# Kernel tuning notes

Hardware: AMD Instinct MI355X
Metric: run time of the kernel (lower is better)

Reference implementation:

```python
import jax, jax.numpy as jnp
import numpy as np

BATCH, N_SITES, BOND, PHYS = 4096, 1024, 32, 2
NOISE = 0.001  # keep trace of long product positive so log() is finite in fp32


def setup_inputs() -> dict:
    key = jax.random.key(0)
    k1, k2 = jax.random.split(key)
    s = jax.random.normal(k1, (BATCH, N_SITES), dtype=jnp.float32)
    # MPS tensor A[p] = I + small noise (same shapes/math as the module's param;
    # identity offset keeps the 1024-matrix product numerically benign)
    A = jnp.eye(BOND, dtype=jnp.float32)[None, :, :] + NOISE * jax.random.normal(
        k2, (PHYS, BOND, BOND), dtype=jnp.float32)
    return {"s": s, "A": A}


def reference(s, A):
    # s: [B, N] float; A: [phys, D, D]
    s_idx = (s > 0).astype(jnp.int32)               # phys_dim == 2 path: [B, N]
    B = s.shape[0]
    D = A.shape[-1]
    init = jnp.broadcast_to(jnp.eye(D, dtype=A.dtype), (B, D, D))

    def contract_site(carry, idx):
        # gather per-sample site matrix [B, D, D], batched matmul
        return jnp.matmul(carry, A[idx]), None

    final_prod, _ = jax.lax.scan(contract_site, init, s_idx.T)  # scan over N sites
    val = jnp.trace(final_prod, axis1=1, axis2=2)               # [B]
    return jnp.log(val)
```

## Files before the change

kernel.cpp:

```cpp
#include <hip/hip_runtime.h>
#include <hip/hip_bf16.h>


#define BATCH   4096
#define N_SITES 1024
#define NKEYS   256
#define NSTEP_H 64

typedef __attribute__((ext_vector_type(8)))  short    short8;
typedef __attribute__((ext_vector_type(16))) float    f32x16;
typedef __attribute__((ext_vector_type(4)))  unsigned uint4v;

static __device__ __forceinline__ unsigned short f32_to_bf16(float f) {
  unsigned u = __builtin_bit_cast(unsigned, f);
  const unsigned rounding = 0x7FFFu + ((u >> 16) & 1u);
  return (unsigned short)((u + rounding) >> 16);
}

static __device__ __forceinline__ unsigned cvt_pk_bf16(float lo, float hi) {
  unsigned r;
  asm("v_cvt_pk_bf16_f32 %0, %1, %2" : "=v"(r) : "v"(lo), "v"(hi));
  return r;
}

__global__ __launch_bounds__(256) void build_table_k(const float* __restrict__ A,
                                                     unsigned short* __restrict__ table) {
  __shared__ float As[2][32][32];
  __shared__ float M[2][32][32];
  const int key = blockIdx.x;
  const int t   = threadIdx.x;

  for (int i = t; i < 2 * 32 * 32; i += 256) ((float*)As)[i] = A[i];

  const int row = t >> 3;
  const int col = (t & 7) << 2;
  __syncthreads();

  {
    const int b0 = key & 1;
    const float4 v = *reinterpret_cast<const float4*>(&As[b0][row][col]);
    *reinterpret_cast<float4*>(&M[0][row][col]) = v;
  }
  __syncthreads();

  int cur = 0;
  for (int i = 1; i < 8; ++i) {
    const int bi = (key >> i) & 1;
    float a0 = 0.f, a1 = 0.f, a2 = 0.f, a3 = 0.f;
    for (int k = 0; k < 32; ++k) {
      const float m  = M[cur][row][k];
      const float4 v = *reinterpret_cast<const float4*>(&As[bi][k][col]);
      a0 += m * v.x; a1 += m * v.y; a2 += m * v.z; a3 += m * v.w;
    }
    M[cur ^ 1][row][col + 0] = a0;
    M[cur ^ 1][row][col + 1] = a1;
    M[cur ^ 1][row][col + 2] = a2;
    M[cur ^ 1][row][col + 3] = a3;
    __syncthreads();
    cur ^= 1;
  }

  const int c    = t >> 7;
  const int l    = (t >> 1) & 63;
  const int e4   = (t & 1) << 2;
  const int rowm = l & 31;
  const int hi   = l >> 5;

  unsigned long long packed = 0;
  for (int e = 0; e < 4; ++e) {
    const int ee = e4 + e;
    const int sg = (ee & 3) + ((ee >> 2) << 3) + (hi << 2) + (c << 4);
    const unsigned short us = f32_to_bf16(M[cur][sg][rowm]);
    packed |= (unsigned long long)us << (16 * e);
  }
  *reinterpret_cast<unsigned long long*>(table + (size_t)key * 1024 + c * 512 + l * 8 + e4) = packed;
}

__global__ __launch_bounds__(256) void mps_chain_k(const float* __restrict__ s,
                                                   const unsigned short* __restrict__ table,
                                                   float* __restrict__ out) {
  const int t    = threadIdx.x;
  const int pair = t >> 7;
  const int wv   = (t >> 6) & 1;
  const int lane = t & 63;
  const int b    = blockIdx.x * 2 + pair;

  __shared__ unsigned char keys[2][128 + 8];
  __shared__ float Ht[2][1024];

  const int kidx = wv * 64 + lane;
  const float4* s4 = reinterpret_cast<const float4*>(s) + (size_t)b * 256 + kidx * 2;
  const float4 va = s4[0];
  const float4 vb = s4[1];
  const unsigned key =
      (va.x > 0.f ? 1u : 0u)  | (va.y > 0.f ? 2u : 0u)  |
      (va.z > 0.f ? 4u : 0u)  | (va.w > 0.f ? 8u : 0u)  |
      (vb.x > 0.f ? 16u : 0u) | (vb.y > 0.f ? 32u : 0u) |
      (vb.z > 0.f ? 64u : 0u) | (vb.w > 0.f ? 128u : 0u);
  keys[pair][kidx] = (unsigned char)key;
  if (t < 16) keys[t >> 3][128 + (t & 7)] = 0;
  __syncthreads();

  const int col = lane & 31;
  const int hi  = lane >> 5;

  f32x16 acc;
#pragma unroll
  for (int r = 0; r < 16; ++r) {
    const int rr = (r & 3) + 8 * (r >> 2) + 4 * hi;
    acc[r] = (rr == col) ? 1.f : 0.f;
  }

  const unsigned char* kw = keys[pair] + wv * NSTEP_H;
  const unsigned long long laneoff = (unsigned long long)lane * 8;

  unsigned kA = kw[0], kB = kw[1];
  unsigned kC = kw[2];
  const unsigned short* e0 = table + (size_t)kA * 1024;
  const unsigned short* e1 = table + (size_t)kB * 1024;
  uint4v c0 = *reinterpret_cast<const uint4v*>(e0 + laneoff);
  uint4v c1 = *reinterpret_cast<const uint4v*>(e0 + 512 + laneoff);
  uint4v n0 = *reinterpret_cast<const uint4v*>(e1 + laneoff);
  uint4v n1 = *reinterpret_cast<const uint4v*>(e1 + 512 + laneoff);

#pragma unroll 4
  for (int j = 0; j < NSTEP_H; ++j) {
    const unsigned short* ef = table + ((size_t)kC << 10);
    const uint4v f0 = *reinterpret_cast<const uint4v*>(ef + laneoff);
    const uint4v f1 = *reinterpret_cast<const uint4v*>(ef + 512 + laneoff);
    kC = kw[j + 3];

    union { unsigned u[4]; short8 v; } B1, B2;
#pragma unroll
    for (int i = 0; i < 4; ++i) {
      B1.u[i] = cvt_pk_bf16(acc[2 * i],     acc[2 * i + 1]);
      B2.u[i] = cvt_pk_bf16(acc[8 + 2 * i], acc[9 + 2 * i]);
    }

    union { uint4v q; short8 v; } ua0, ua1;
    ua0.q = c0; ua1.q = c1;

    f32x16 z;
#pragma unroll
    for (int r = 0; r < 16; ++r) z[r] = 0.f;

    f32x16 t1 = __builtin_amdgcn_mfma_f32_32x32x16_bf16(ua0.v, B1.v, z, 0, 0, 0);
    acc = __builtin_amdgcn_mfma_f32_32x32x16_bf16(ua1.v, B2.v, t1, 0, 0, 0);
    asm("" : "+v"(acc));

    c0 = n0; c1 = n1; n0 = f0; n1 = f1;
  }

  if (wv == 1) {
#pragma unroll
    for (int r = 0; r < 16; ++r) {
      const int a = (r & 3) + 8 * (r >> 2) + 4 * hi;
      Ht[pair][col * 32 + ((a + col) & 31)] = acc[r];
    }
  }
  __syncthreads();
  if (wv == 0) {
    float dot = 0.f;
#pragma unroll
    for (int r = 0; r < 16; ++r) {
      const int k = (r & 3) + 8 * (r >> 2) + 4 * hi;
      dot += acc[r] * Ht[pair][k * 32 + ((col + k) & 31)];
    }
#pragma unroll
    for (int off = 32; off > 0; off >>= 1) dot += __shfl_down(dot, off, 64);
    if (lane == 0) out[b] = logf(dot);
  }
}

extern "C" void kernel_launch(void* const* d_in, const int* in_sizes, int n_in,
                              void* d_out, int out_size, void* d_ws, size_t ws_size,
                              hipStream_t stream) {
  const float* s = (const float*)d_in[0];
  const float* A = (const float*)d_in[1];
  float* out = (float*)d_out;
  unsigned short* table = (unsigned short*)d_ws;

  build_table_k<<<NKEYS, 256, 0, stream>>>(A, table);
  mps_chain_k<<<BATCH / 2, 256, 0, stream>>>(s, table, out);
}
```

Baseline: 118.7 us.

## Interleave two independent sample chains per wave to hide MFMA latency

Each wave now advances two samples' matrix chains at once, interleaving their MFMA and bf16 conversion steps so the two dependency chains overlap. Each block handles four samples instead of two, and the grid is halved. The aim is to hide the serial MFMA-to-convert latency of a single chain. In exchange each wave holds more registers and there are fewer blocks, which may lower occupancy.

```diff
diff --git a/kernel.cpp b/kernel.cpp
--- a/kernel.cpp
+++ b/kernel.cpp
@@ -80,95 +80,126 @@
                                                    const unsigned short* __restrict__ table,
                                                    float* __restrict__ out) {
   const int t    = threadIdx.x;
-  const int pair = t >> 7;
-  const int wv   = (t >> 6) & 1;
+  const int wave = t >> 6;
   const int lane = t & 63;
-  const int b    = blockIdx.x * 2 + pair;
-
-  __shared__ unsigned char keys[2][128 + 8];
-  __shared__ float Ht[2][1024];
-
-  const int kidx = wv * 64 + lane;
-  const float4* s4 = reinterpret_cast<const float4*>(s) + (size_t)b * 256 + kidx * 2;
-  const float4 va = s4[0];
-  const float4 vb = s4[1];
-  const unsigned key =
-      (va.x > 0.f ? 1u : 0u)  | (va.y > 0.f ? 2u : 0u)  |
-      (va.z > 0.f ? 4u : 0u)  | (va.w > 0.f ? 8u : 0u)  |
-      (vb.x > 0.f ? 16u : 0u) | (vb.y > 0.f ? 32u : 0u) |
-      (vb.z > 0.f ? 64u : 0u) | (vb.w > 0.f ? 128u : 0u);
-  keys[pair][kidx] = (unsigned char)key;
-  if (t < 16) keys[t >> 3][128 + (t & 7)] = 0;
+  const int half = wave & 1;
+  const int bA   = (wave >> 1) * 2;
+  const int bB   = bA + 1;
+
+  __shared__ unsigned char keys[4][136];
+  __shared__ float Ht[4][1024];
+
+#pragma unroll
+  for (int g = t; g < 512; g += 256) {
+    const int kb   = g >> 7;
+    const int kidx = g & 127;
+    const int bg   = blockIdx.x * 4 + kb;
+    const float4* s4 = reinterpret_cast<const float4*>(s) + (size_t)bg * 256 + kidx * 2;
+    const float4 va = s4[0];
+    const float4 vb = s4[1];
+    const unsigned key =
+        (va.x > 0.f ? 1u : 0u)  | (va.y > 0.f ? 2u : 0u)  |
+        (va.z > 0.f ? 4u : 0u)  | (va.w > 0.f ? 8u : 0u)  |
+        (vb.x > 0.f ? 16u : 0u) | (vb.y > 0.f ? 32u : 0u) |
+        (vb.z > 0.f ? 64u : 0u) | (vb.w > 0.f ? 128u : 0u);
+    keys[kb][kidx] = (unsigned char)key;
+  }
+  if (t < 32) keys[t >> 3][128 + (t & 7)] = 0;
   __syncthreads();
 
   const int col = lane & 31;
   const int hi  = lane >> 5;
 
-  f32x16 acc;
+  f32x16 accA, accB;
 #pragma unroll
   for (int r = 0; r < 16; ++r) {
     const int rr = (r & 3) + 8 * (r >> 2) + 4 * hi;
-    acc[r] = (rr == col) ? 1.f : 0.f;
-  }
-
-  const unsigned char* kw = keys[pair] + wv * NSTEP_H;
+    const float v = (rr == col) ? 1.f : 0.f;
+    accA[r] = v; accB[r] = v;
+  }
+
+  const unsigned char* kwA = &keys[bA][half * NSTEP_H];
+  const unsigned char* kwB = &keys[bB][half * NSTEP_H];
   const unsigned long long laneoff = (unsigned long long)lane * 8;
 
-  unsigned kA = kw[0], kB = kw[1];
-  unsigned kC = kw[2];
-  const unsigned short* e0 = table + (size_t)kA * 1024;
-  const unsigned short* e1 = table + (size_t)kB * 1024;
-  uint4v c0 = *reinterpret_cast<const uint4v*>(e0 + laneoff);
-  uint4v c1 = *reinterpret_cast<const uint4v*>(e0 + 512 + laneoff);
-  uint4v n0 = *reinterpret_cast<const uint4v*>(e1 + laneoff);
-  uint4v n1 = *reinterpret_cast<const uint4v*>(e1 + 512 + laneoff);
-
-#pragma unroll 4
+  const unsigned short* eA0 = table + ((size_t)kwA[0] << 10);
+  const unsigned short* eA1 = table + ((size_t)kwA[1] << 10);
+  const unsigned short* eB0 = table + ((size_t)kwB[0] << 10);
+  const unsigned short* eB1 = table + ((size_t)kwB[1] << 10);
+  unsigned kCA = kwA[2], kCB = kwB[2];
+  uint4v cA0 = *reinterpret_cast<const uint4v*>(eA0 + laneoff);
+  uint4v cA1 = *reinterpret_cast<const uint4v*>(eA0 + 512 + laneoff);
+  uint4v nA0 = *reinterpret_cast<const uint4v*>(eA1 + laneoff);
+  uint4v nA1 = *reinterpret_cast<const uint4v*>(eA1 + 512 + laneoff);
+  uint4v cB0 = *reinterpret_cast<const uint4v*>(eB0 + laneoff);
+  uint4v cB1 = *reinterpret_cast<const uint4v*>(eB0 + 512 + laneoff);
+  uint4v nB0 = *reinterpret_cast<const uint4v*>(eB1 + laneoff);
+  uint4v nB1 = *reinterpret_cast<const uint4v*>(eB1 + 512 + laneoff);
+
+#pragma unroll 2
   for (int j = 0; j < NSTEP_H; ++j) {
-    const unsigned short* ef = table + ((size_t)kC << 10);
-    const uint4v f0 = *reinterpret_cast<const uint4v*>(ef + laneoff);
-    const uint4v f1 = *reinterpret_cast<const uint4v*>(ef + 512 + laneoff);
-    kC = kw[j + 3];
-
-    union { unsigned u[4]; short8 v; } B1, B2;
+    const unsigned short* efA = table + ((size_t)kCA << 10);
+    const uint4v fA0 = *reinterpret_cast<const uint4v*>(efA + laneoff);
+    const uint4v fA1 = *reinterpret_cast<const uint4v*>(efA + 512 + laneoff);
+    kCA = kwA[j + 3];
+    const unsigned short* efB = table + ((size_t)kCB << 10);
+    const uint4v fB0 = *reinterpret_cast<const uint4v*>(efB + laneoff);
+    const uint4v fB1 = *reinterpret_cast<const uint4v*>(efB + 512 + laneoff);
+    kCB = kwB[j + 3];
+
+    f32x16 z;
+#pragma unroll
+    for (int r = 0; r < 16; ++r) z[r] = 0.f;
+
+    union { unsigned u[4]; short8 v; } BA1, BA2, BB1, BB2;
 #pragma unroll
     for (int i = 0; i < 4; ++i) {
-      B1.u[i] = cvt_pk_bf16(acc[2 * i],     acc[2 * i + 1]);
-      B2.u[i] = cvt_pk_bf16(acc[8 + 2 * i], acc[9 + 2 * i]);
-    }
-
-    union { uint4v q; short8 v; } ua0, ua1;
-    ua0.q = c0; ua1.q = c1;
-
-    f32x16 z;
-#pragma unroll
-    for (int r = 0; r < 16; ++r) z[r] = 0.f;
-
-    f32x16 t1 = __builtin_amdgcn_mfma_f32_32x32x16_bf16(ua0.v, B1.v, z, 0, 0, 0);
-    acc = __builtin_amdgcn_mfma_f32_32x32x16_bf16(ua1.v, B2.v, t1, 0, 0, 0);
-    asm("" : "+v"(acc));
-
-    c0 = n0; c1 = n1; n0 = f0; n1 = f1;
-  }
-
-  if (wv == 1) {
+      BA1.u[i] = cvt_pk_bf16(accA[2 * i],     accA[2 * i + 1]);
+      BA2.u[i] = cvt_pk_bf16(accA[8 + 2 * i], accA[9 + 2 * i]);
+      BB1.u[i] = cvt_pk_bf16(accB[2 * i],     accB[2 * i + 1]);
+      BB2.u[i] = cvt_pk_bf16(accB[8 + 2 * i], accB[9 + 2 * i]);
+    }
+
+    union { uint4v q; short8 v; } uA0, uA1, uB0, uB1;
+    uA0.q = cA0; uA1.q = cA1; uB0.q = cB0; uB1.q = cB1;
+
+    f32x16 tA = __builtin_amdgcn_mfma_f32_32x32x16_bf16(uA0.v, BA1.v, z, 0, 0, 0);
+    f32x16 tB = __builtin_amdgcn_mfma_f32_32x32x16_bf16(uB0.v, BB1.v, z, 0, 0, 0);
+    accA = __builtin_amdgcn_mfma_f32_32x32x16_bf16(uA1.v, BA2.v, tA, 0, 0, 0);
+    accB = __builtin_amdgcn_mfma_f32_32x32x16_bf16(uB1.v, BB2.v, tB, 0, 0, 0);
+
+    cA0 = nA0; cA1 = nA1; nA0 = fA0; nA1 = fA1;
+    cB0 = nB0; cB1 = nB1; nB0 = fB0; nB1 = fB1;
+  }
+
+  if (half == 1) {
 #pragma unroll
     for (int r = 0; r < 16; ++r) {
       const int a = (r & 3) + 8 * (r >> 2) + 4 * hi;
-      Ht[pair][col * 32 + ((a + col) & 31)] = acc[r];
-    }
-  }
-  __syncthreads();
-  if (wv == 0) {
-    float dot = 0.f;
+      const int slot = col * 32 + ((a + col) & 31);
+      Ht[bA][slot] = accA[r];
+      Ht[bB][slot] = accB[r];
+    }
+  }
+  __syncthreads();
+  if (half == 0) {
+    float d0 = 0.f, d1 = 0.f;
 #pragma unroll
     for (int r = 0; r < 16; ++r) {
       const int k = (r & 3) + 8 * (r >> 2) + 4 * hi;
-      dot += acc[r] * Ht[pair][k * 32 + ((col + k) & 31)];
-    }
-#pragma unroll
-    for (int off = 32; off > 0; off >>= 1) dot += __shfl_down(dot, off, 64);
-    if (lane == 0) out[b] = logf(dot);
+      const int slot = k * 32 + ((col + k) & 31);
+      d0 += accA[r] * Ht[bA][slot];
+      d1 += accB[r] * Ht[bB][slot];
+    }
+#pragma unroll
+    for (int off = 32; off > 0; off >>= 1) {
+      d0 += __shfl_down(d0, off, 64);
+      d1 += __shfl_down(d1, off, 64);
+    }
+    if (lane == 0) {
+      out[blockIdx.x * 4 + bA] = logf(d0);
+      out[blockIdx.x * 4 + bB] = logf(d1);
+    }
   }
 }
 
@@ -181,5 +212,5 @@
   unsigned short* table = (unsigned short*)d_ws;
 
   build_table_k<<<NKEYS, 256, 0, stream>>>(A, table);
-  mps_chain_k<<<BATCH / 2, 256, 0, stream>>>(s, table, out);
-}
+  mps_chain_k<<<BATCH / 4, 256, 0, stream>>>(s, table, out);
+}
```

Result: no change. 116.4 us (-1.9%).

## Split each sample's chain across four waves and merge partial products

Applied to the files above, without the earlier changes.

Each sample's chain of 128 grouped-site matrices is now split across four waves of 32 steps each instead of two waves of 64. The previous split used two samples per block. The four partial products are combined in a tree: waves 0 and 2 each multiply in their neighbour's product through LDS, then the trace is taken as a dot product. This halves the serial MFMA dependency chain per wave and sets a launch-bounds occupancy hint. In exchange it adds an extra bf16 rounding, extra LDS traffic and syncs, and twice as many blocks.

```diff
diff --git a/kernel.cpp b/kernel.cpp
--- a/kernel.cpp
+++ b/kernel.cpp
@@ -5,7 +5,7 @@
 #define BATCH   4096
 #define N_SITES 1024
 #define NKEYS   256
-#define NSTEP_H 64
+#define NSTEP_Q 32
 
 typedef __attribute__((ext_vector_type(8)))  short    short8;
 typedef __attribute__((ext_vector_type(16))) float    f32x16;
@@ -76,29 +76,31 @@
   *reinterpret_cast<unsigned long long*>(table + (size_t)key * 1024 + c * 512 + l * 8 + e4) = packed;
 }
 
-__global__ __launch_bounds__(256) void mps_chain_k(const float* __restrict__ s,
-                                                   const unsigned short* __restrict__ table,
-                                                   float* __restrict__ out) {
+__global__ __launch_bounds__(256, 8) void mps_chain_k(const float* __restrict__ s,
+                                                      const unsigned short* __restrict__ table,
+                                                      float* __restrict__ out) {
   const int t    = threadIdx.x;
-  const int pair = t >> 7;
-  const int wv   = (t >> 6) & 1;
+  const int wv   = t >> 6;
   const int lane = t & 63;
-  const int b    = blockIdx.x * 2 + pair;
-
-  __shared__ unsigned char keys[2][128 + 8];
-  __shared__ float Ht[2][1024];
-
-  const int kidx = wv * 64 + lane;
-  const float4* s4 = reinterpret_cast<const float4*>(s) + (size_t)b * 256 + kidx * 2;
-  const float4 va = s4[0];
-  const float4 vb = s4[1];
-  const unsigned key =
-      (va.x > 0.f ? 1u : 0u)  | (va.y > 0.f ? 2u : 0u)  |
-      (va.z > 0.f ? 4u : 0u)  | (va.w > 0.f ? 8u : 0u)  |
-      (vb.x > 0.f ? 16u : 0u) | (vb.y > 0.f ? 32u : 0u) |
-      (vb.z > 0.f ? 64u : 0u) | (vb.w > 0.f ? 128u : 0u);
-  keys[pair][kidx] = (unsigned char)key;
-  if (t < 16) keys[t >> 3][128 + (t & 7)] = 0;
+  const int b    = blockIdx.x;
+
+  __shared__ unsigned char keys[136];
+  __shared__ float Qt1[1024];
+  __shared__ float Qt3[1024];
+  __shared__ float Ht[1024];
+
+  if (t < 128) {
+    const float4* s4 = reinterpret_cast<const float4*>(s) + (size_t)b * 256 + t * 2;
+    const float4 va = s4[0];
+    const float4 vb = s4[1];
+    keys[t] =
+        (unsigned char)((va.x > 0.f ? 1u : 0u)  | (va.y > 0.f ? 2u : 0u)  |
+                        (va.z > 0.f ? 4u : 0u)  | (va.w > 0.f ? 8u : 0u)  |
+                        (vb.x > 0.f ? 16u : 0u) | (vb.y > 0.f ? 32u : 0u) |
+                        (vb.z > 0.f ? 64u : 0u) | (vb.w > 0.f ? 128u : 0u));
+  } else if (t < 136) {
+    keys[t] = 0;
+  }
   __syncthreads();
 
   const int col = lane & 31;
@@ -111,24 +113,24 @@
     acc[r] = (rr == col) ? 1.f : 0.f;
   }
 
-  const unsigned char* kw = keys[pair] + wv * NSTEP_H;
+  const unsigned char* kw = keys + wv * NSTEP_Q;
   const unsigned long long laneoff = (unsigned long long)lane * 8;
 
-  unsigned kA = kw[0], kB = kw[1];
-  unsigned kC = kw[2];
-  const unsigned short* e0 = table + (size_t)kA * 1024;
-  const unsigned short* e1 = table + (size_t)kB * 1024;
+  const unsigned short* e0 = table + ((size_t)kw[0] << 10);
   uint4v c0 = *reinterpret_cast<const uint4v*>(e0 + laneoff);
   uint4v c1 = *reinterpret_cast<const uint4v*>(e0 + 512 + laneoff);
-  uint4v n0 = *reinterpret_cast<const uint4v*>(e1 + laneoff);
-  uint4v n1 = *reinterpret_cast<const uint4v*>(e1 + 512 + laneoff);
-
-#pragma unroll 4
-  for (int j = 0; j < NSTEP_H; ++j) {
-    const unsigned short* ef = table + ((size_t)kC << 10);
+  unsigned kN = kw[1];
+
+#pragma unroll 2
+  for (int j = 0; j < NSTEP_Q; ++j) {
+    const unsigned short* ef = table + ((size_t)kN << 10);
     const uint4v f0 = *reinterpret_cast<const uint4v*>(ef + laneoff);
     const uint4v f1 = *reinterpret_cast<const uint4v*>(ef + 512 + laneoff);
-    kC = kw[j + 3];
+    kN = kw[j + 2];
+
+    f32x16 z;
+#pragma unroll
+    for (int r = 0; r < 16; ++r) z[r] = 0.f;
 
     union { unsigned u[4]; short8 v; } B1, B2;
 #pragma unroll
@@ -137,25 +139,59 @@
       B2.u[i] = cvt_pk_bf16(acc[8 + 2 * i], acc[9 + 2 * i]);
     }
 
-    union { uint4v q; short8 v; } ua0, ua1;
-    ua0.q = c0; ua1.q = c1;
+    union { uint4v q; short8 v; } u0, u1;
+    u0.q = c0; u1.q = c1;
+
+    f32x16 t1 = __builtin_amdgcn_mfma_f32_32x32x16_bf16(u0.v, B1.v, z, 0, 0, 0);
+    acc = __builtin_amdgcn_mfma_f32_32x32x16_bf16(u1.v, B2.v, t1, 0, 0, 0);
+
+    c0 = f0; c1 = f1;
+  }
+
+  if (wv == 1 || wv == 3) {
+    float* qp = (wv == 1) ? Qt1 : Qt3;
+#pragma unroll
+    for (int r = 0; r < 16; ++r) {
+      const int x = (r & 3) + 8 * (r >> 2) + 4 * hi;
+      qp[x * 32 + ((col + x) & 31)] = acc[r];
+    }
+  }
+  __syncthreads();
+
+  if (wv == 0 || wv == 2) {
+    const float* qp = (wv == 0) ? Qt1 : Qt3;
+    union { unsigned u[4]; short8 v; } A1, A2;
+#pragma unroll
+    for (int i = 0; i < 4; ++i) {
+      const int e0i = 2 * i, e1i = 2 * i + 1;
+      const int sgA = (e0i & 3) + 8 * (e0i >> 2) + 4 * hi;
+      const int sgB = (e1i & 3) + 8 * (e1i >> 2) + 4 * hi;
+      A1.u[i] = cvt_pk_bf16(qp[col * 32 + ((sgA + col) & 31)],
+                            qp[col * 32 + ((sgB + col) & 31)]);
+      A2.u[i] = cvt_pk_bf16(qp[col * 32 + (((sgA + 16) + col) & 31)],
+                            qp[col * 32 + (((sgB + 16) + col) & 31)]);
+    }
+
+    union { unsigned u[4]; short8 v; } B1, B2;
+#pragma unroll
+    for (int i = 0; i < 4; ++i) {
+      B1.u[i] = cvt_pk_bf16(acc[2 * i],     acc[2 * i + 1]);
+      B2.u[i] = cvt_pk_bf16(acc[8 + 2 * i], acc[9 + 2 * i]);
+    }
 
     f32x16 z;
 #pragma unroll
     for (int r = 0; r < 16; ++r) z[r] = 0.f;
 
-    f32x16 t1 = __builtin_amdgcn_mfma_f32_32x32x16_bf16(ua0.v, B1.v, z, 0, 0, 0);
-    acc = __builtin_amdgcn_mfma_f32_32x32x16_bf16(ua1.v, B2.v, t1, 0, 0, 0);
-    asm("" : "+v"(acc));
-
-    c0 = n0; c1 = n1; n0 = f0; n1 = f1;
-  }
-
-  if (wv == 1) {
+    f32x16 t1 = __builtin_amdgcn_mfma_f32_32x32x16_bf16(A1.v, B1.v, z, 0, 0, 0);
+    acc = __builtin_amdgcn_mfma_f32_32x32x16_bf16(A2.v, B2.v, t1, 0, 0, 0);
+  }
+
+  if (wv == 2) {
 #pragma unroll
     for (int r = 0; r < 16; ++r) {
       const int a = (r & 3) + 8 * (r >> 2) + 4 * hi;
-      Ht[pair][col * 32 + ((a + col) & 31)] = acc[r];
+      Ht[col * 32 + ((a + col) & 31)] = acc[r];
     }
   }
   __syncthreads();
@@ -164,7 +200,7 @@
 #pragma unroll
     for (int r = 0; r < 16; ++r) {
       const int k = (r & 3) + 8 * (r >> 2) + 4 * hi;
-      dot += acc[r] * Ht[pair][k * 32 + ((col + k) & 31)];
+      dot += acc[r] * Ht[k * 32 + ((col + k) & 31)];
     }
 #pragma unroll
     for (int off = 32; off > 0; off >>= 1) dot += __shfl_down(dot, off, 64);
@@ -181,5 +217,5 @@
   unsigned short* table = (unsigned short*)d_ws;
 
   build_table_k<<<NKEYS, 256, 0, stream>>>(A, table);
-  mps_chain_k<<<BATCH / 2, 256, 0, stream>>>(s, table, out);
-}
+  mps_chain_k<<<BATCH, 256, 0, stream>>>(s, table, out);
+}
```

Measured after the change: 110.8 us. 1.07x faster.
